# Performance work log

Measured on AMD Instinct MI355X. Metric: run time of the kernel, lower is better.

Reference implementation:

```python
import jax, jax.numpy as jnp
import numpy as np

K = 16
NS = [2048, 512, 128]

def _knn(q, r, k):
    # q: [B,M,3] query centers, r: [B,N,3] reference points -> (idx [B,M,k], sqdist [B,M,k])
    d2 = (jnp.sum(q * q, -1)[:, :, None] + jnp.sum(r * r, -1)[:, None, :]
          - 2.0 * jnp.einsum('bmd,bnd->bmn', q, r))
    neg, idx = jax.lax.top_k(-d2, k)
    return idx, jnp.maximum(-neg, 0.0)

def _gather(feat, idx):
    # feat [B,N,C], idx [B,M,k] -> [B,M,k,C]
    return jax.vmap(lambda f, i: f[i])(feat, idx)

def _down(x, pos, n, W1, b1, W2, b2):
    # PointNet++-style TransitionDown: sample n centers, kNN group, rel-pos concat, shared MLP, max-pool
    centers = pos[:, :n]
    idx, _ = _knn(centers, pos, K)
    rel = _gather(pos, idx) - centers[:, :, None, :]           # [B,n,K,3]
    feat = jnp.concatenate([rel, _gather(x, idx)], -1)          # [B,n,K,C+3]
    h = jax.nn.relu(feat @ W1 + b1) @ W2 + b2                   # last_act=False
    return jnp.max(h, axis=2), centers

def _up(xc, pc, prv_feat, prv_pos, W, b):
    # TransitionUp: 3-NN inverse-distance interpolation + skip concat + pointwise conv1d
    idx, d2 = _knn(prv_pos, pc, 3)
    w = 1.0 / (d2 + 1e-8)
    w = w / jnp.sum(w, -1, keepdims=True)
    interp = jnp.sum(_gather(xc, idx) * w[..., None], axis=2)   # [B,Nprv,Cc]
    cat = jnp.concatenate([interp, prv_feat], -1)
    return jax.nn.relu(cat @ W + b)

def setup_inputs() -> dict:
    key = jax.random.key(0)
    ks = jax.random.split(key, 16)
    p = lambda k, s: jax.random.normal(k, s, jnp.float32) * 0.02
    B, N = 4, 8192
    return {
        'x': jax.random.normal(ks[0], (B, N, 3), jnp.float32),
        'pos': jax.random.uniform(ks[1], (B, N, 3), jnp.float32),
        'd0_W1': p(ks[2], (6, 128)),   'd0_b1': jnp.zeros((128,), jnp.float32),
        'd0_W2': p(ks[3], (128, 128)), 'd0_b2': jnp.zeros((128,), jnp.float32),
        'd1_W1': p(ks[4], (131, 256)), 'd1_b1': jnp.zeros((256,), jnp.float32),
        'd1_W2': p(ks[5], (256, 256)), 'd1_b2': jnp.zeros((256,), jnp.float32),
        'd2_W1': p(ks[6], (259, 512)), 'd2_b1': jnp.zeros((512,), jnp.float32),
        'd2_W2': p(ks[7], (512, 512)), 'd2_b2': jnp.zeros((512,), jnp.float32),
        'u0_W': p(ks[8], (768, 256)),  'u0_b': jnp.zeros((256,), jnp.float32),
        'u1_W': p(ks[9], (384, 128)),  'u1_b': jnp.zeros((128,), jnp.float32),
        'u2_W': p(ks[10], (134, 128)), 'u2_b': jnp.zeros((128,), jnp.float32),
        'f_W1': p(ks[11], (128, 128)), 'f_b1': jnp.zeros((128,), jnp.float32),
        'f_W2': p(ks[12], (128, 128)), 'f_b2': jnp.zeros((128,), jnp.float32),
    }

def reference(x, pos, d0_W1, d0_b1, d0_W2, d0_b2, d1_W1, d1_b1, d1_W2, d1_b2,
              d2_W1, d2_b1, d2_W2, d2_b2, u0_W, u0_b, u1_W, u1_b, u2_W, u2_b,
              f_W1, f_b1, f_W2, f_b2):
    pos0, x0 = pos, x
    # encoder (transition-down) with cached (pos, x) per scale
    x1, pos1 = _down(x0, pos0, NS[0], d0_W1, d0_b1, d0_W2, d0_b2)
    x2, pos2 = _down(x1, pos1, NS[1], d1_W1, d1_b1, d1_W2, d1_b2)
    x3, pos3 = _down(x2, pos2, NS[2], d2_W1, d2_b1, d2_W2, d2_b2)
    # decoder (transition-up) consuming the cache in reverse; last level concats raw pos to skip feat
    up = _up(x3, pos3, x2, pos2, u0_W, u0_b)
    up = _up(up, pos2, x1, pos1, u1_W, u1_b)
    prv0 = jnp.concatenate([x0, pos0], -1)
    up = _up(up, pos1, prv0, pos0, u2_W, u2_b)
    # feat_map_layer_out: two pointwise conv1d layers, last_act=False
    out = jax.nn.relu(up @ f_W1 + f_b1) @ f_W2 + f_b2
    return (out, pos0)
```

## Files before the change

### kernel.cpp

```cpp
#include <hip/hip_runtime.h>

#define NFULL 8192
#define BATCH 4

typedef unsigned long long u64;
typedef unsigned int u32;
typedef __attribute__((ext_vector_type(8))) short bf8_t;
typedef __attribute__((ext_vector_type(4))) float f4_t;

__device__ __forceinline__ u32 fbias(float f) {
  u32 u = __float_as_uint(f);
  return (u & 0x80000000u) ? ~u : (u | 0x80000000u);
}
__device__ __forceinline__ float funbias(u32 b) {
  u32 u = (b & 0x80000000u) ? (b & 0x7fffffffu) : ~b;
  return __uint_as_float(u);
}
__device__ __forceinline__ short f2bf(float f) {
  u32 u = __float_as_uint(f);
  u32 r = u + 0x7FFFu + ((u >> 16) & 1u);
  return (short)(r >> 16);
}

__global__ __launch_bounds__(256) void build_grids_kernel(
    const float* __restrict__ pos, float4* __restrict__ sortedA,
    int* __restrict__ csA, float4* __restrict__ sortedB, int* __restrict__ csB,
    float4* __restrict__ sortedC, int* __restrict__ csC) {
  __shared__ int cnt[4096];
  __shared__ int partial[256];
  int which = blockIdx.y, b = blockIdx.x, t = threadIdx.x;
  int NREF = (which == 0) ? 8192 : (which == 1) ? 2048 : 512;
  int GR = (which == 0) ? 16 : 8;
  int NC = GR * GR * GR;
  float4* sorted = ((which == 0) ? sortedA : (which == 1) ? sortedB : sortedC)
                   + (size_t)b * NREF;
  int* cs = ((which == 0) ? csA + b * 4097 : (which == 1) ? csB + b * 513
                                           : csC + b * 513);
  const float* pb = pos + (size_t)b * NFULL * 3;
  for (int c = t; c < NC; c += 256) cnt[c] = 0;
  __syncthreads();
  for (int p = t; p < NREF; p += 256) {
    float x = pb[p * 3 + 0], y = pb[p * 3 + 1], z = pb[p * 3 + 2];
    int cx = min(max((int)(x * GR), 0), GR - 1);
    int cy = min(max((int)(y * GR), 0), GR - 1);
    int cz = min(max((int)(z * GR), 0), GR - 1);
    atomicAdd(&cnt[(cz * GR + cy) * GR + cx], 1);
  }
  __syncthreads();
  int chunk = (NC + 255) / 256;
  int s = 0;
  for (int i = 0; i < chunk; ++i) {
    int c = t * chunk + i;
    if (c < NC) s += cnt[c];
  }
  partial[t] = s;
  __syncthreads();
  if (t == 0) {
    int run = 0;
    for (int i = 0; i < 256; ++i) { int v = partial[i]; partial[i] = run; run += v; }
  }
  __syncthreads();
  int run = partial[t];
  for (int i = 0; i < chunk; ++i) {
    int c = t * chunk + i;
    if (c < NC) { int v = cnt[c]; cnt[c] = run; run += v; }
  }
  __syncthreads();
  for (int c = t; c < NC; c += 256) cs[c] = cnt[c];
  if (t == 0) cs[NC] = NREF;
  __syncthreads();
  for (int p = t; p < NREF; p += 256) {
    float x = pb[p * 3 + 0], y = pb[p * 3 + 1], z = pb[p * 3 + 2];
    int cx = min(max((int)(x * GR), 0), GR - 1);
    int cy = min(max((int)(y * GR), 0), GR - 1);
    int cz = min(max((int)(z * GR), 0), GR - 1);
    int slot = atomicAdd(&cnt[(cz * GR + cy) * GR + cx], 1);
    sorted[slot] = make_float4(x, y, z, __uint_as_float((u32)p));
  }
}

template<int SL>
__device__ __forceinline__ void group_insert(u32 m16, u64 ck, int slot,
                                             u64& val, u64& tau) {
  if (m16) {
    while (m16) {
      int src = __ffs(m16) - 1;
      m16 &= m16 - 1;
      u64 c = __shfl((unsigned long long)ck, src, 16);
      u64 prev = __shfl_up((unsigned long long)val, 1, SL);
      if (slot == 0) prev = 0ull;
      val = (val <= c) ? val : ((prev <= c) ? c : prev);
    }
    tau = __shfl((unsigned long long)val, SL - 1, SL);
  }
}

template<int SL>
__device__ __forceinline__ void first_round_sort(u64 ck, int gl,
                                                 u64& val, u64& tau) {
  u64 v = ck;
#pragma unroll
  for (int size = 2; size <= 16; size <<= 1) {
#pragma unroll
    for (int stride = size >> 1; stride > 0; stride >>= 1) {
      u64 other = __shfl_xor((unsigned long long)v, stride, 16);
      bool ddd = ((gl & size) == 0);
      bool takeMin = (((gl & stride) == 0) == ddd);
      u64 mn = (v <= other) ? v : other;
      u64 mx = (v <= other) ? other : v;
      v = takeMin ? mn : mx;
    }
  }
  if (SL < 16) v = __shfl((unsigned long long)v, gl & (SL - 1), 16);
  val = v;
  tau = __shfl((unsigned long long)v, SL - 1, SL);
}

__device__ __forceinline__ void lane_insert3(u64 ck, u64& v0, u64& v1, u64& v2) {
  u64 a = (v0 <= ck) ? v0 : ck;
  u64 bb = (v0 <= ck) ? ck : v0;
  v0 = a;
  u64 c = (v1 <= bb) ? v1 : bb;
  u64 d = (v1 <= bb) ? bb : v1;
  v1 = c;
  v2 = (v2 <= d) ? v2 : d;
}

__device__ __forceinline__ void merge3(u64 v0, u64 v1, u64 v2,
                                       u64& o0, u64& o1, u64& o2) {
  u64 h = v0;
  int hc = 0;
  u64 outs[3];
#pragma unroll
  for (int k = 0; k < 3; ++k) {
    u64 m = h;
#pragma unroll
    for (int st = 1; st < 16; st <<= 1) {
      u64 o = __shfl_xor((unsigned long long)m, st, 16);
      m = (m <= o) ? m : o;
    }
    outs[k] = m;
    if (h == m) { ++hc; h = (hc == 1) ? v1 : ((hc == 2) ? v2 : ~0ull); }
  }
  o0 = outs[0]; o1 = outs[1]; o2 = outs[2];
}

__device__ __forceinline__ void scan_range3(const float4* __restrict__ sb,
    int s, int e, float qx, float qy, float qz, float qq,
    int gl, u64& v0, u64& v1, u64& v2) {
  for (int t0 = s; t0 < e; t0 += 16) {
    int j = t0 + gl;
    if (j < e) {
      float4 P = sb[j];
      float rr = P.x * P.x + P.y * P.y + P.z * P.z;
      float d2 = qq + rr - 2.0f * (qx * P.x + qy * P.y + qz * P.z);
      u64 ck = ((u64)fbias(d2) << 32) | (u32)__float_as_uint(P.w);
      lane_insert3(ck, v0, v1, v2);
    }
  }
}

template<int SL>
__device__ __forceinline__ void scan_range(const float4* __restrict__ sb,
    int s, int e, float qx, float qy, float qz, float qq,
    int g, int gl, int slot, u64& val, u64& tau) {
  for (int t0 = s; t0 < e; t0 += 16) {
    int j = t0 + gl;
    u64 ck = ~0ull;
    if (j < e) {
      float4 P = sb[j];
      float rr = P.x * P.x + P.y * P.y + P.z * P.z;
      float d2 = qq + rr - 2.0f * (qx * P.x + qy * P.y + qz * P.z);
      ck = ((u64)fbias(d2) << 32) | (u32)__float_as_uint(P.w);
    }
    u64 full = __ballot(ck < tau);
    u32 m16 = (u32)((full >> (g * 16)) & 0xFFFFull);
    group_insert<SL>(m16, ck, slot, val, tau);
  }
}


template<int SL, int KOUT, int GR, int R, int NREF>
__device__ __forceinline__ void knn_tail(
    const float4* __restrict__ sb, const int* __restrict__ cs,
    float qx, float qy, float qz, float qq,
    int ix, int iy, int iz, int x0, int x1, int y0, int y1, int z0, int z1,
    int g, int gl, int slot, u64& val, u64& tau) {
  const float h = 1.0f / GR;
  float m = 1e30f;
  if (x0 > 0)      m = fminf(m, qx - x0 * h);
  if (x1 < GR - 1) m = fminf(m, (x1 + 1) * h - qx);
  if (y0 > 0)      m = fminf(m, qy - y0 * h);
  if (y1 < GR - 1) m = fminf(m, (y1 + 1) * h - qy);
  if (z0 > 0)      m = fminf(m, qz - z0 * h);
  if (z1 < GR - 1) m = fminf(m, (z1 + 1) * h - qz);
  float bound = m * m;
  u64 kv = __shfl((unsigned long long)val, KOUT - 1, SL);
  float kth_d2 = funbias((u32)(kv >> 32));
  if (!(kth_d2 < bound)) {
    int X0 = max(ix - (R + 1), 0), X1 = min(ix + (R + 1), GR - 1);
    int Y0 = max(iy - (R + 1), 0), Y1 = min(iy + (R + 1), GR - 1);
    int Z0 = max(iz - (R + 1), 0), Z1 = min(iz + (R + 1), GR - 1);
    int NY2 = Y1 - Y0 + 1;
    int nrow2 = (Z1 - Z0 + 1) * NY2;
    for (int rr2 = 0; rr2 < nrow2; ++rr2) {
      int zz = Z0 + rr2 / NY2, yy = Y0 + rr2 % NY2;
      int c0 = (zz * GR + yy) * GR;
      bool mid = (zz >= z0 && zz <= z1 && yy >= y0 && yy <= y1);
      int s1 = cs[c0 + X0];
      int e1 = mid ? cs[c0 + x0] : cs[c0 + X1 + 1];
      scan_range<SL>(sb, s1, e1, qx, qy, qz, qq, g, gl, slot, val, tau);
      if (mid) {
        int s2 = cs[c0 + x1 + 1];
        int e2 = cs[c0 + X1 + 1];
        scan_range<SL>(sb, s2, e2, qx, qy, qz, qq, g, gl, slot, val, tau);
      }
    }
    x0 = X0; x1 = X1; y0 = Y0; y1 = Y1; z0 = Z0; z1 = Z1;
    m = 1e30f;
    if (x0 > 0)      m = fminf(m, qx - x0 * h);
    if (x1 < GR - 1) m = fminf(m, (x1 + 1) * h - qx);
    if (y0 > 0)      m = fminf(m, qy - y0 * h);
    if (y1 < GR - 1) m = fminf(m, (y1 + 1) * h - qy);
    if (z0 > 0)      m = fminf(m, qz - z0 * h);
    if (z1 < GR - 1) m = fminf(m, (z1 + 1) * h - qz);
    bound = m * m;
    kv = __shfl((unsigned long long)val, KOUT - 1, SL);
    kth_d2 = funbias((u32)(kv >> 32));
    if (!(kth_d2 < bound)) {
      for (int t0 = 0; t0 < NREF; t0 += 16) {
        int j = t0 + gl;
        u64 ck = ~0ull;
        if (j < NREF) {
          float4 P = sb[j];
          int cx = min(max((int)(P.x * GR), 0), GR - 1);
          int cy = min(max((int)(P.y * GR), 0), GR - 1);
          int cz = min(max((int)(P.z * GR), 0), GR - 1);
          bool inbox = (cx >= x0 && cx <= x1 && cy >= y0 && cy <= y1 &&
                        cz >= z0 && cz <= z1);
          if (!inbox) {
            float rr = P.x * P.x + P.y * P.y + P.z * P.z;
            float d2 = qq + rr - 2.0f * (qx * P.x + qy * P.y + qz * P.z);
            ck = ((u64)fbias(d2) << 32) | (u32)__float_as_uint(P.w);
          }
        }
        u64 full = __ballot(ck < tau);
        u32 m16 = (u32)((full >> (g * 16)) & 0xFFFFull);
        group_insert<SL>(m16, ck, slot, val, tau);
      }
    }
  }
}

template<int GR, int R, int NREF>
__device__ __forceinline__ void knn_tail3(
    const float4* __restrict__ sb, const int* __restrict__ cs,
    float qx, float qy, float qz, float qq,
    int ix, int iy, int iz, int x0, int x1, int y0, int y1, int z0, int z1,
    int gl, u64& v0, u64& v1, u64& v2, u64& o0, u64& o1, u64& o2) {
  const float h = 1.0f / GR;
  float m = 1e30f;
  if (x0 > 0)      m = fminf(m, qx - x0 * h);
  if (x1 < GR - 1) m = fminf(m, (x1 + 1) * h - qx);
  if (y0 > 0)      m = fminf(m, qy - y0 * h);
  if (y1 < GR - 1) m = fminf(m, (y1 + 1) * h - qy);
  if (z0 > 0)      m = fminf(m, qz - z0 * h);
  if (z1 < GR - 1) m = fminf(m, (z1 + 1) * h - qz);
  float bound = m * m;
  merge3(v0, v1, v2, o0, o1, o2);
  float kth_d2 = funbias((u32)(o2 >> 32));
  if (!(kth_d2 < bound)) {
    int X0 = max(ix - (R + 1), 0), X1 = min(ix + (R + 1), GR - 1);
    int Y0 = max(iy - (R + 1), 0), Y1 = min(iy + (R + 1), GR - 1);
    int Z0 = max(iz - (R + 1), 0), Z1 = min(iz + (R + 1), GR - 1);
    int NY2 = Y1 - Y0 + 1;
    int nrow2 = (Z1 - Z0 + 1) * NY2;
    for (int rr2 = 0; rr2 < nrow2; ++rr2) {
      int zz = Z0 + rr2 / NY2, yy = Y0 + rr2 % NY2;
      int c0 = (zz * GR + yy) * GR;
      bool mid = (zz >= z0 && zz <= z1 && yy >= y0 && yy <= y1);
      int s1 = cs[c0 + X0];
      int e1 = mid ? cs[c0 + x0] : cs[c0 + X1 + 1];
// ... 203 lines not shown

__device__ void knn_brute3_dev(int vbx,
    const float* __restrict__ pos, int Nref, int Mq,
    int* __restrict__ oidx, float* __restrict__ od2) {
  int b = blockIdx.y;
  int wv = threadIdx.x >> 6, lane = threadIdx.x & 63;
  int g = lane >> 4, gl = lane & 15;
  int q = vbx * 16 + wv * 4 + g;
  const float* pb = pos + (size_t)b * NFULL * 3;
  float qx = pb[q * 3 + 0], qy = pb[q * 3 + 1], qz = pb[q * 3 + 2];
  float qq = qx * qx + qy * qy + qz * qz;

  u64 v0 = ~0ull, v1 = ~0ull, v2 = ~0ull;
  for (int j = gl; j < Nref; j += 16) {
    float rx = pb[j * 3 + 0];
    float ry = pb[j * 3 + 1];
    float rz = pb[j * 3 + 2];
    float rr = rx * rx + ry * ry + rz * rz;
    float d2 = qq + rr - 2.0f * (qx * rx + qy * ry + qz * rz);
    u64 ck = ((u64)fbias(d2) << 32) | (u32)j;
    lane_insert3(ck, v0, v1, v2);
  }
  u64 o0, o1, o2;
  merge3(v0, v1, v2, o0, o1, o2);

  if (gl < 3) {
    u64 val = (gl == 0) ? o0 : ((gl == 1) ? o1 : o2);
    size_t base = ((size_t)b * Mq + q) * 3;
    oidx[base + gl] = (int)(u32)val;
    od2[base + gl] = fmaxf(funbias((u32)(val >> 32)), 0.0f);
  }
}

template<int SL, int KOUT, int GR, int R, int NREF>
__device__ void knn_grid_flat32_dev(int vbx,
    const float* __restrict__ pos, const float4* __restrict__ sorted,
    const int* __restrict__ cellStart, int csStride, int Mq,
    int* __restrict__ oidx, float* __restrict__ od2) {
  int b = blockIdx.y;
  int wv = threadIdx.x >> 6, lane = threadIdx.x & 63;
  int g = lane >> 4, gl = lane & 15;
  int q = vbx * 16 + wv * 4 + g;
  const float* pb = pos + (size_t)b * NFULL * 3;
  const float4* sb = sorted + (size_t)b * NREF;
  const int* cs = cellStart + b * csStride;
  float qx = pb[q * 3 + 0], qy = pb[q * 3 + 1], qz = pb[q * 3 + 2];
  float qq = qx * qx + qy * qy + qz * qz;
  int ix = min(max((int)(qx * GR), 0), GR - 1);
  int iy = min(max((int)(qy * GR), 0), GR - 1);
  int iz = min(max((int)(qz * GR), 0), GR - 1);
  int x0 = max(ix - R, 0), x1 = min(ix + R, GR - 1);
  int y0 = max(iy - R, 0), y1 = min(iy + R, GR - 1);
  int z0 = max(iz - R, 0), z1 = min(iz + R, GR - 1);

  int ny = y1 - y0 + 1;
  int nrow = (z1 - z0 + 1) * ny;
  int sLo = 0, lenLo = 0, sHi = 0, lenHi = 0;
  if (gl < nrow) {
    int zz = z0 + gl / ny, yy = y0 + gl % ny;
    int c0 = (zz * GR + yy) * GR + x0;
    sLo = cs[c0]; lenLo = cs[c0 + (x1 - x0) + 1] - sLo;
  }
  {
    int i2 = gl + 16;
    if (i2 < nrow) {
      int zz = z0 + i2 / ny, yy = y0 + i2 % ny;
      int c0 = (zz * GR + yy) * GR + x0;
      sHi = cs[c0]; lenHi = cs[c0 + (x1 - x0) + 1] - sHi;
    }
  }
  int pLo = lenLo, pHi = lenHi;
#pragma unroll
  for (int st = 1; st < 16; st <<= 1) {
    int o = __shfl_up(pLo, st, 16);
    if (gl >= st) pLo += o;
    int o2 = __shfl_up(pHi, st, 16);
    if (gl >= st) pHi += o2;
  }
  int tot16 = __shfl(pLo, 15, 16);
  pHi += tot16;
  int T = __shfl(pHi, 15, 16);
  pLo -= lenLo; pHi -= lenHi;
  int dLo = sLo - pLo, dHi = sHi - pHi;
  if (gl >= nrow) pLo = 0x7fffffff;
  if (gl + 16 >= nrow) pHi = 0x7fffffff;

  int slot = gl & (SL - 1);
  u64 val, tau;

  {
    int v = gl;
    int r = 0;
#pragma unroll
    for (int st = 16; st >= 1; st >>= 1) {
      int j = r + st;
      int pcL = __shfl(pLo, j & 15, 16);
      int pcH = __shfl(pHi, j & 15, 16);
      int pc = (j < 16) ? pcL : pcH;
      if (v >= pc) r = j;
    }
    int dL = __shfl(dLo, r & 15, 16);
    int dH = __shfl(dHi, r & 15, 16);
    int addr = v + ((r < 16) ? dL : dH);
    u64 ck = ~0ull;
    if (v < T) {
      float4 P = sb[addr];
      float rr = P.x * P.x + P.y * P.y + P.z * P.z;
      float d2 = qq + rr - 2.0f * (qx * P.x + qy * P.y + qz * P.z);
      ck = ((u64)fbias(d2) << 32) | (u32)__float_as_uint(P.w);
    }
    first_round_sort<SL>(ck, gl, val, tau);
  }

  for (int v0 = 16; v0 < T; v0 += 16) {
    int v = v0 + gl;
    int r = 0;
#pragma unroll
    for (int st = 16; st >= 1; st >>= 1) {
      int j = r + st;
      int pcL = __shfl(pLo, j & 15, 16);
      int pcH = __shfl(pHi, j & 15, 16);
      int pc = (j < 16) ? pcL : pcH;
      if (v >= pc) r = j;
    }
    int dL = __shfl(dLo, r & 15, 16);
    int dH = __shfl(dHi, r & 15, 16);
    int addr = v + ((r < 16) ? dL : dH);
    u64 ck = ~0ull;
    if (v < T) {
      float4 P = sb[addr];
      float rr = P.x * P.x + P.y * P.y + P.z * P.z;
      float d2 = qq + rr - 2.0f * (qx * P.x + qy * P.y + qz * P.z);
      ck = ((u64)fbias(d2) << 32) | (u32)__float_as_uint(P.w);
    }
    u64 full = __ballot(ck < tau);
    u32 m16 = (u32)((full >> (g * 16)) & 0xFFFFull);
    group_insert<SL>(m16, ck, slot, val, tau);
  }

  knn_tail<SL, KOUT, GR, R, NREF>(sb, cs, qx, qy, qz, qq,
      ix, iy, iz, x0, x1, y0, y1, z0, z1, g, gl, slot, val, tau);

  if (gl < KOUT) {
    size_t base = ((size_t)b * Mq + q) * KOUT;
    oidx[base + gl] = (int)(u32)val;
    if (od2) od2[base + gl] = fmaxf(funbias((u32)(val >> 32)), 0.0f);
  }
}

template<int SL, int KOUT>
__device__ void knn_brute_dev(int vbx,
    const float* __restrict__ pos, int Nref, int Mq,
    int* __restrict__ oidx, float* __restrict__ od2) {
  int b = blockIdx.y;
  int wv = threadIdx.x >> 6, lane = threadIdx.x & 63;
  int g = lane >> 4, gl = lane & 15;
  int q = vbx * 16 + wv * 4 + g;
  const float* pb = pos + (size_t)b * NFULL * 3;
  float qx = pb[q * 3 + 0], qy = pb[q * 3 + 1], qz = pb[q * 3 + 2];
  float qq = qx * qx + qy * qy + qz * qz;

  int slot = gl & (SL - 1);
  u64 val, tau;

  {
    int j = gl;
    float rx = pb[j * 3 + 0];
    float ry = pb[j * 3 + 1];
    float rz = pb[j * 3 + 2];
    float rr = rx * rx + ry * ry + rz * rz;
    float d2 = qq + rr - 2.0f * (qx * rx + qy * ry + qz * rz);
    u64 ck = ((u64)fbias(d2) << 32) | (u32)j;
    first_round_sort<SL>(ck, gl, val, tau);
  }

  for (int t0 = 16; t0 < Nref; t0 += 16) {
    int j = t0 + gl;
    float rx = pb[j * 3 + 0];
    float ry = pb[j * 3 + 1];
    float rz = pb[j * 3 + 2];
    float rr = rx * rx + ry * ry + rz * rz;
    float d2 = qq + rr - 2.0f * (qx * rx + qy * ry + qz * rz);
    u64 ck = ((u64)fbias(d2) << 32) | (u32)j;
    u64 full = __ballot(ck < tau);
    u32 m16 = (u32)((full >> (g * 16)) & 0xFFFFull);
    group_insert<SL>(m16, ck, slot, val, tau);
  }

  if (gl < KOUT) {
    size_t base = ((size_t)b * Mq + q) * KOUT;
    oidx[base + gl] = (int)(u32)val;
    if (od2) od2[base + gl] = fmaxf(funbias((u32)(val >> 32)), 0.0f);
  }
}

__global__ __launch_bounds__(256) void knn_all_kernel(
    const float* __restrict__ pos,
    const float4* __restrict__ sortedA, const int* __restrict__ csA,
    const float4* __restrict__ sortedB, const int* __restrict__ csB,
    const float4* __restrict__ sortedC, const int* __restrict__ csC,
    int* __restrict__ idx0, int* __restrict__ idx1, int* __restrict__ idx2,
    int* __restrict__ idxu0, float* __restrict__ d2u0,
    int* __restrict__ idxu1, float* __restrict__ d2u1,
    int* __restrict__ idxu2, float* __restrict__ d2u2) {
  int bx = blockIdx.x;
  if (bx < 8)
    knn_brute_dev<16, 16>(bx, pos, 512, 128, idx2, nullptr);
  else if (bx < 40)
    knn_grid_flat32_dev<16, 16, 8, 2, 2048>(bx - 8, pos, sortedB, csB, 513, 512, idx1, nullptr);
  else if (bx < 168)
    knn_grid_flat32_dev<16, 16, 16, 2, 8192>(bx - 40, pos, sortedA, csA, 4097, 2048, idx0, nullptr);
  else if (bx < 296)
    knn_grid_flat32_3_dev<8, 2, 512>(bx - 168, pos, sortedC, csC, 513, 2048, idxu1, d2u1);
  else if (bx < 808)
    knn_grid_flat3_dev<8, 1, 2048>(bx - 296, pos, sortedB, csB, 513, 8192, idxu2, d2u2);
  else
    knn_brute3_dev(bx - 808, pos, 128, 512, idxu0, d2u0);
}

__device__ __forceinline__ void pack_tile_rt(const float* __restrict__ W,
                                             short* __restrict__ outp,
                                             int KDIM, int N, int tile, int lane) {
  int NT = N >> 4;
  int kt = tile / NT, nt = tile - kt * NT;
  int n = nt * 16 + (lane & 15);
  int k0 = kt * 32 + (lane >> 4) * 8;
  bf8_t v;
#pragma unroll
  for (int j = 0; j < 8; ++j) {
    int k = k0 + j;
    v[j] = (k < KDIM) ? f2bf(W[(size_t)k * N + n]) : (short)0;
  }
  *(bf8_t*)(outp + ((size_t)tile * 64 + lane) * 8) = v;
}

__global__ __launch_bounds__(64) void pack_copy_all_kernel(
    const float* d0W1, short* d0W1p, const float* d0W2, short* d0W2p,
    const float* d1W1, short* d1W1p, const float* d1W2, short* d1W2p,
    const float* d2W1, short* d2W1p, const float* d2W2, short* d2W2p,
    const float* u2W, short* u2Wp, const float* fW1, short* fW1p,
    const float* fW2, short* fW2p,
    const float* u0W, short* u0Wp, const float* u1W, short* u1Wp,
    const float* pos, float* posOut) {
  int blk = blockIdx.x, lane = threadIdx.x;
  if      (blk < 8)    pack_tile_rt(d0W1, d0W1p, 6, 128, blk, lane);
  else if (blk < 40)   pack_tile_rt(d0W2, d0W2p, 128, 128, blk - 8, lane);
  else if (blk < 120)  pack_tile_rt(d1W1, d1W1p, 131, 256, blk - 40, lane);
  else if (blk < 248)  pack_tile_rt(d1W2, d1W2p, 256, 256, blk - 120, lane);
  else if (blk < 536)  pack_tile_rt(d2W1, d2W1p, 259, 512, blk - 248, lane);
  else if (blk < 1048) pack_tile_rt(d2W2, d2W2p, 512, 512, blk - 536, lane);
  else if (blk < 1088) pack_tile_rt(u2W, u2Wp, 134, 128, blk - 1048, lane);
  else if (blk < 1120) pack_tile_rt(fW1, fW1p, 128, 128, blk - 1088, lane);
  else if (blk < 1152) pack_tile_rt(fW2, fW2p, 128, 128, blk - 1120, lane);
  else if (blk < 1536) pack_tile_rt(u0W, u0Wp, 768, 256, blk - 1152, lane);
  else if (blk < 1632) pack_tile_rt(u1W, u1Wp, 384, 128, blk - 1536, lane);
  else {
    int base = (blk - 1632) * 256;
#pragma unroll
    for (int j = 0; j < 4; ++j) {
      int i = base + lane + j * 64;
      posOut[i] = pos[i];
    }
  }
}

template<int FEAT, int CIN, int CHID, int FPAD, int QB, int WAVES>
__global__ __launch_bounds__(64 * WAVES) void down_mfma_kernel(
    const float* __restrict__ pos, const float* __restrict__ xin,
    const int* __restrict__ idx,
    const short* __restrict__ W1p, const float* __restrict__ b1,
    const short* __restrict__ W2p, const float* __restrict__ b2,
    float* __restrict__ out, int n, int nprev) {
  const int KT1 = FPAD / 32, NT1 = CHID / 16;
  const int KT2 = CHID / 32, NT2 = CHID / 16;
  __shared__ short sFeat[QB][16][FPAD + 8];
  __shared__ short sH1[QB][16][CHID + 8];
  __shared__ int sIdx[QB][16];
  __shared__ float sCtr[QB][3];
  int b = blockIdx.y, q0 = blockIdx.x * QB;
  int t = threadIdx.x;
  int lane = t & 63, wv = t >> 6;
  const float* pb = pos + (size_t)b * NFULL * 3;
  const float* xb = xin + (size_t)b * nprev * CIN;
  if (t < QB * 16)
    sIdx[t >> 4][t & 15] = idx[((size_t)b * n + q0 + (t >> 4)) * 16 + (t & 15)];
  if (t < QB * 3) sCtr[t / 3][t % 3] = pb[(q0 + t / 3) * 3 + (t % 3)];
  __syncthreads();
  for (int e = t; e < QB * 16 * FPAD; e += 64 * WAVES) {
    int k = e / FPAD, c = e - k * FPAD;
    int qq = k >> 4, kk = k & 15;
    float v = 0.f;
    if (c < 3) v = pb[sIdx[qq][kk] * 3 + c] - sCtr[qq][c];
    else if (c < FEAT) v = xb[(size_t)sIdx[qq][kk] * CIN + (c - 3)];
    sFeat[qq][kk][c] = f2bf(v);
  }
  __syncthreads();
// ... 268 lines not shown
  float* x2    = (float*)(ws + 4194304);
  float* x3    = (float*)(ws + 6291456);
  float* up0o  = (float*)(ws + 7340032);
  float* up1o  = (float*)(ws + 9437184);
  int*   idx0  = (int*)  (ws + 13631488);
  int*   idx1  = (int*)  (ws + 14155776);
  int*   idx2  = (int*)  (ws + 14286848);
  float4* sortedC = (float4*)(ws + 14319616);
  int*    csC     = (int*)   (ws + 14352384);
  int*   idxu0 = (int*)  (ws + 14843904);
  float* d2u0  = (float*)(ws + 14868480);
  int*   idxu1 = (int*)  (ws + 14893056);
  float* d2u1  = (float*)(ws + 14991360);
  int*   idxu2 = (int*)  (ws + 15089664);
  float* d2u2  = (float*)(ws + 15482880);
  short* d1W1p = (short*)(ws + 15876096);
  short* d1W2p = (short*)(ws + 15958016);
  short* d2W1p = (short*)(ws + 16089088);
  short* d2W2p = (short*)(ws + 16384000);
  short* d0W1p = (short*)(ws + 16908288);
  short* d0W2p = (short*)(ws + 16916480);
  float4* sortedA = (float4*)(ws + 16949248);
  int*    csA     = (int*)   (ws + 17473536);
  float4* sortedB = (float4*)(ws + 17539136);
  int*    csB     = (int*)   (ws + 17670208);
  short* u2Wp  = (short*)(ws + 17697920);
  short* fW1p  = (short*)(ws + 17738880);
  short* fW2p  = (short*)(ws + 17771648);

  float* out = (float*)d_out;
  short* u0Wp = (short*)out;
  short* u1Wp = (short*)(out + 98304);

  pack_copy_all_kernel<<<dim3(2016), 64, 0, stream>>>(
      d0W1, d0W1p, d0W2, d0W2p, d1W1, d1W1p, d1W2, d1W2p,
      d2W1, d2W1p, d2W2, d2W2p, u2W, u2Wp, fW1, fW1p, fW2, fW2p,
      u0W, u0Wp, u1W, u1Wp,
      pos, out + (size_t)BATCH * NFULL * 128);
  build_grids_kernel<<<dim3(BATCH, 3), 256, 0, stream>>>(
      pos, sortedA, csA, sortedB, csB, sortedC, csC);

  knn_all_kernel<<<dim3(840, BATCH), 256, 0, stream>>>(
      pos, sortedA, csA, sortedB, csB, sortedC, csC,
      idx0, idx1, idx2,
      idxu0, d2u0, idxu1, d2u1, idxu2, d2u2);

  down_mfma_kernel<6, 3, 128, 32, 4, 4><<<dim3(512, BATCH), 256, 0, stream>>>(
      pos, x, idx0, d0W1p, d0b1, d0W2p, d0b2, x1, 2048, 8192);
  down_mfma_kernel<131, 128, 256, 160, 4, 8><<<dim3(128, BATCH), 512, 0, stream>>>(
      pos, x1, idx1, d1W1p, d1b1, d1W2p, d1b2, x2, 512, 2048);
  down_mfma_kernel<259, 256, 512, 288, 2, 8><<<dim3(64, BATCH), 512, 0, stream>>>(
      pos, x2, idx2, d2W1p, d2b1, d2W2p, d2b2, x3, 128, 512);

  up_mfma_kernel<512, 256, 256, 4><<<dim3(32, BATCH), 256, 0, stream>>>(
      x3, 128, idxu0, d2u0, x2, u0Wp, u0b, up0o, 512);
  up_mfma_kernel<256, 128, 128, 2><<<dim3(128, BATCH), 128, 0, stream>>>(
      up0o, 512, idxu1, d2u1, x1, u1Wp, u1b, up1o, 2048);
  up2f_mfma_kernel<<<dim3(512, BATCH), 128, 0, stream>>>(
      up1o, idxu2, d2u2, x, pos, u2Wp, u2b, fW1p, fb1, fW2p, fb2, out);
}
```

Measured before the change: 299.9 us.

## Use 32-lane kNN groups and merge grid build with weight packing kernel

The K=16 kNN searches now give each query 32 lanes instead of 16. Each scan step therefore evaluates 32 candidates, and the per-row prefix scan spans all 32 lanes, removing the Lo/Hi split. The separate weight-pack/pos-copy kernel and grid-build kernel are fused into one pre_kernel, saving a launch. The cost is fewer queries per wave, more blocks, and potentially more serial insert iterations per ballot.

```diff
diff --git a/kernel.cpp b/kernel.cpp
--- a/kernel.cpp
+++ b/kernel.cpp
@@ -22,13 +22,74 @@
   return (short)(r >> 16);
 }
 
-__global__ __launch_bounds__(256) void build_grids_kernel(
+__device__ __forceinline__ void pack_tile_rt(const float* __restrict__ W,
+                                             short* __restrict__ outp,
+                                             int KDIM, int N, int tile, int lane) {
+  int NT = N >> 4;
+  int kt = tile / NT, nt = tile - kt * NT;
+  int n = nt * 16 + (lane & 15);
+  int k0 = kt * 32 + (lane >> 4) * 8;
+  bf8_t v;
+#pragma unroll
+  for (int j = 0; j < 8; ++j) {
+    int k = k0 + j;
+    v[j] = (k < KDIM) ? f2bf(W[(size_t)k * N + n]) : (short)0;
+  }
+  *(bf8_t*)(outp + ((size_t)tile * 64 + lane) * 8) = v;
+}
+
+__device__ void pack_dispatch(int blk, int lane,
+    const float* d0W1, short* d0W1p, const float* d0W2, short* d0W2p,
+    const float* d1W1, short* d1W1p, const float* d1W2, short* d1W2p,
+    const float* d2W1, short* d2W1p, const float* d2W2, short* d2W2p,
+    const float* u2W, short* u2Wp, const float* fW1, short* fW1p,
+    const float* fW2, short* fW2p,
+    const float* u0W, short* u0Wp, const float* u1W, short* u1Wp,
+    const float* pos, float* posOut) {
+  if      (blk < 8)    pack_tile_rt(d0W1, d0W1p, 6, 128, blk, lane);
+  else if (blk < 40)   pack_tile_rt(d0W2, d0W2p, 128, 128, blk - 8, lane);
+  else if (blk < 120)  pack_tile_rt(d1W1, d1W1p, 131, 256, blk - 40, lane);
+  else if (blk < 248)  pack_tile_rt(d1W2, d1W2p, 256, 256, blk - 120, lane);
+  else if (blk < 536)  pack_tile_rt(d2W1, d2W1p, 259, 512, blk - 248, lane);
+  else if (blk < 1048) pack_tile_rt(d2W2, d2W2p, 512, 512, blk - 536, lane);
+  else if (blk < 1088) pack_tile_rt(u2W, u2Wp, 134, 128, blk - 1048, lane);
+  else if (blk < 1120) pack_tile_rt(fW1, fW1p, 128, 128, blk - 1088, lane);
+  else if (blk < 1152) pack_tile_rt(fW2, fW2p, 128, 128, blk - 1120, lane);
+  else if (blk < 1536) pack_tile_rt(u0W, u0Wp, 768, 256, blk - 1152, lane);
+  else if (blk < 1632) pack_tile_rt(u1W, u1Wp, 384, 128, blk - 1536, lane);
+  else {
+    int base = (blk - 1632) * 256;
+#pragma unroll
+    for (int j = 0; j < 4; ++j) {
+      int i = base + lane + j * 64;
+      posOut[i] = pos[i];
+    }
+  }
+}
+
+__global__ __launch_bounds__(256) void pre_kernel(
     const float* __restrict__ pos, float4* __restrict__ sortedA,
     int* __restrict__ csA, float4* __restrict__ sortedB, int* __restrict__ csB,
-    float4* __restrict__ sortedC, int* __restrict__ csC) {
+    float4* __restrict__ sortedC, int* __restrict__ csC,
+    const float* d0W1, short* d0W1p, const float* d0W2, short* d0W2p,
+    const float* d1W1, short* d1W1p, const float* d1W2, short* d1W2p,
+    const float* d2W1, short* d2W1p, const float* d2W2, short* d2W2p,
+    const float* u2W, short* u2Wp, const float* fW1, short* fW1p,
+    const float* fW2, short* fW2p,
+    const float* u0W, short* u0Wp, const float* u1W, short* u1Wp,
+    float* posOut) {
   __shared__ int cnt[4096];
   __shared__ int partial[256];
-  int which = blockIdx.y, b = blockIdx.x, t = threadIdx.x;
+  int bx = blockIdx.x, t = threadIdx.x;
+  if (bx >= 12) {
+    int tt = (bx - 12) * 4 + (t >> 6);
+    pack_dispatch(tt, t & 63,
+        d0W1, d0W1p, d0W2, d0W2p, d1W1, d1W1p, d1W2, d1W2p,
+        d2W1, d2W1p, d2W2, d2W2p, u2W, u2Wp, fW1, fW1p, fW2, fW2p,
+        u0W, u0Wp, u1W, u1Wp, pos, posOut);
+    return;
+  }
+  int which = bx >> 2, b = bx & 3;
   int NREF = (which == 0) ? 8192 : (which == 1) ? 2048 : 512;
   int GR = (which == 0) ? 16 : 8;
   int NC = GR * GR * GR;
@@ -79,31 +140,29 @@
   }
 }
 
-template<int SL>
-__device__ __forceinline__ void group_insert(u32 m16, u64 ck, int slot,
-                                             u64& val, u64& tau) {
-  if (m16) {
-    while (m16) {
-      int src = __ffs(m16) - 1;
-      m16 &= m16 - 1;
-      u64 c = __shfl((unsigned long long)ck, src, 16);
-      u64 prev = __shfl_up((unsigned long long)val, 1, SL);
-      if (slot == 0) prev = 0ull;
+__device__ __forceinline__ void group_insert_g32(u32 m32, u64 ck, int slot16,
+                                                 u64& val, u64& tau) {
+  if (m32) {
+    while (m32) {
+      int src = __ffs(m32) - 1;
+      m32 &= m32 - 1;
+      u64 c = __shfl((unsigned long long)ck, src, 32);
+      u64 prev = __shfl_up((unsigned long long)val, 1, 16);
+      if (slot16 == 0) prev = 0ull;
       val = (val <= c) ? val : ((prev <= c) ? c : prev);
     }
-    tau = __shfl((unsigned long long)val, SL - 1, SL);
-  }
-}
-
-template<int SL>
-__device__ __forceinline__ void first_round_sort(u64 ck, int gl,
-                                                 u64& val, u64& tau) {
+    tau = __shfl((unsigned long long)val, 15, 16);
+  }
+}
+
+__device__ __forceinline__ void first_round_sort32(u64 ck, int gl,
+                                                   u64& val, u64& tau) {
   u64 v = ck;
 #pragma unroll
-  for (int size = 2; size <= 16; size <<= 1) {
+  for (int size = 2; size <= 32; size <<= 1) {
 #pragma unroll
     for (int stride = size >> 1; stride > 0; stride >>= 1) {
-      u64 other = __shfl_xor((unsigned long long)v, stride, 16);
+      u64 other = __shfl_xor((unsigned long long)v, stride, 32);
       bool ddd = ((gl & size) == 0);
       bool takeMin = (((gl & stride) == 0) == ddd);
       u64 mn = (v <= other) ? v : other;
@@ -111,60 +170,14 @@
       v = takeMin ? mn : mx;
     }
   }
-  if (SL < 16) v = __shfl((unsigned long long)v, gl & (SL - 1), 16);
-  val = v;
-  tau = __shfl((unsigned long long)v, SL - 1, SL);
-}
-
-__device__ __forceinline__ void lane_insert3(u64 ck, u64& v0, u64& v1, u64& v2) {
-  u64 a = (v0 <= ck) ? v0 : ck;
-  u64 bb = (v0 <= ck) ? ck : v0;
-  v0 = a;
-  u64 c = (v1 <= bb) ? v1 : bb;
-  u64 d = (v1 <= bb) ? bb : v1;
-  v1 = c;
-  v2 = (v2 <= d) ? v2 : d;
-}
-
-__device__ __forceinline__ void merge3(u64 v0, u64 v1, u64 v2,
-                                       u64& o0, u64& o1, u64& o2) {
-  u64 h = v0;
-  int hc = 0;
-  u64 outs[3];
-#pragma unroll
-  for (int k = 0; k < 3; ++k) {
-    u64 m = h;
-#pragma unroll
-    for (int st = 1; st < 16; st <<= 1) {
-      u64 o = __shfl_xor((unsigned long long)m, st, 16);
-      m = (m <= o) ? m : o;
-    }
-    outs[k] = m;
-    if (h == m) { ++hc; h = (hc == 1) ? v1 : ((hc == 2) ? v2 : ~0ull); }
-  }
-  o0 = outs[0]; o1 = outs[1]; o2 = outs[2];
-}
-
-__device__ __forceinline__ void scan_range3(const float4* __restrict__ sb,
+  val = __shfl((unsigned long long)v, gl & 15, 32);
+  tau = __shfl((unsigned long long)val, 15, 16);
+}
+
+__device__ __forceinline__ void scan_range_g32(const float4* __restrict__ sb,
     int s, int e, float qx, float qy, float qz, float qq,
-    int gl, u64& v0, u64& v1, u64& v2) {
-  for (int t0 = s; t0 < e; t0 += 16) {
-    int j = t0 + gl;
-    if (j < e) {
-      float4 P = sb[j];
-      float rr = P.x * P.x + P.y * P.y + P.z * P.z;
-      float d2 = qq + rr - 2.0f * (qx * P.x + qy * P.y + qz * P.z);
-      u64 ck = ((u64)fbias(d2) << 32) | (u32)__float_as_uint(P.w);
-      lane_insert3(ck, v0, v1, v2);
-    }
-  }
-}
-
-template<int SL>
-__device__ __forceinline__ void scan_range(const float4* __restrict__ sb,
-    int s, int e, float qx, float qy, float qz, float qq,
-    int g, int gl, int slot, u64& val, u64& tau) {
-  for (int t0 = s; t0 < e; t0 += 16) {
+    int g32, int gl, int slot16, u64& val, u64& tau) {
+  for (int t0 = s; t0 < e; t0 += 32) {
     int j = t0 + gl;
     u64 ck = ~0ull;
     if (j < e) {
@@ -174,18 +187,17 @@
       ck = ((u64)fbias(d2) << 32) | (u32)__float_as_uint(P.w);
     }
     u64 full = __ballot(ck < tau);
-    u32 m16 = (u32)((full >> (g * 16)) & 0xFFFFull);
-    group_insert<SL>(m16, ck, slot, val, tau);
-  }
-}
-
-
-template<int SL, int KOUT, int GR, int R, int NREF>
-__device__ __forceinline__ void knn_tail(
+    u32 m32 = (u32)(full >> (g32 * 32));
+    group_insert_g32(m32, ck, slot16, val, tau);
+  }
+}
+
+template<int GR, int R, int NREF>
+__device__ __forceinline__ void knn_tail16_g32(
     const float4* __restrict__ sb, const int* __restrict__ cs,
     float qx, float qy, float qz, float qq,
     int ix, int iy, int iz, int x0, int x1, int y0, int y1, int z0, int z1,
-    int g, int gl, int slot, u64& val, u64& tau) {
+    int g32, int gl, int slot16, u64& val, u64& tau) {
   const float h = 1.0f / GR;
   float m = 1e30f;
   if (x0 > 0)      m = fminf(m, qx - x0 * h);
@@ -195,8 +207,7 @@
   if (z0 > 0)      m = fminf(m, qz - z0 * h);
   if (z1 < GR - 1) m = fminf(m, (z1 + 1) * h - qz);
   float bound = m * m;
-  u64 kv = __shfl((unsigned long long)val, KOUT - 1, SL);
-  float kth_d2 = funbias((u32)(kv >> 32));
+  float kth_d2 = funbias((u32)(tau >> 32));
   if (!(kth_d2 < bound)) {
     int X0 = max(ix - (R + 1), 0), X1 = min(ix + (R + 1), GR - 1);
     int Y0 = max(iy - (R + 1), 0), Y1 = min(iy + (R + 1), GR - 1);
@@ -209,11 +220,11 @@
       bool mid = (zz >= z0 && zz <= z1 && yy >= y0 && yy <= y1);
       int s1 = cs[c0 + X0];
       int e1 = mid ? cs[c0 + x0] : cs[c0 + X1 + 1];
-      scan_range<SL>(sb, s1, e1, qx, qy, qz, qq, g, gl, slot, val, tau);
+      scan_range_g32(sb, s1, e1, qx, qy, qz, qq, g32, gl, slot16, val, tau);
       if (mid) {
         int s2 = cs[c0 + x1 + 1];
         int e2 = cs[c0 + X1 + 1];
-        scan_range<SL>(sb, s2, e2, qx, qy, qz, qq, g, gl, slot, val, tau);
+        scan_range_g32(sb, s2, e2, qx, qy, qz, qq, g32, gl, slot16, val, tau);
       }
     }
     x0 = X0; x1 = X1; y0 = Y0; y1 = Y1; z0 = Z0; z1 = Z1;
@@ -225,10 +236,9 @@
     if (z0 > 0)      m = fminf(m, qz - z0 * h);
     if (z1 < GR - 1) m = fminf(m, (z1 + 1) * h - qz);
     bound = m * m;
-    kv = __shfl((unsigned long long)val, KOUT - 1, SL);
-    kth_d2 = funbias((u32)(kv >> 32));
+    kth_d2 = funbias((u32)(tau >> 32));
     if (!(kth_d2 < bound)) {
-      for (int t0 = 0; t0 < NREF; t0 += 16) {
+      for (int t0 = 0; t0 < NREF; t0 += 32) {
         int j = t0 + gl;
         u64 ck = ~0ull;
         if (j < NREF) {
@@ -245,9 +255,189 @@
           }
         }
         u64 full = __ballot(ck < tau);
-        u32 m16 = (u32)((full >> (g * 16)) & 0xFFFFull);
-        group_insert<SL>(m16, ck, slot, val, tau);
+        u32 m32 = (u32)(full >> (g32 * 32));
+        group_insert_g32(m32, ck, slot16, val, tau);
       }
+    }
+  }
+}
+
+template<int GR, int R, int NREF>
+__device__ void knn_grid16_g32_dev(int vbx,
+    const float* __restrict__ pos, const float4* __restrict__ sorted,
+    const int* __restrict__ cellStart, int csStride, int Mq,
+    int* __restrict__ oidx) {
+  int b = blockIdx.y;
+  int wv = threadIdx.x >> 6, lane = threadIdx.x & 63;
+  int g32 = lane >> 5, gl = lane & 31;
+  int q = vbx * 8 + wv * 2 + g32;
+  const float* pb = pos + (size_t)b * NFULL * 3;
+  const float4* sb = sorted + (size_t)b * NREF;
+  const int* cs = cellStart + b * csStride;
+  float qx = pb[q * 3 + 0], qy = pb[q * 3 + 1], qz = pb[q * 3 + 2];
+  float qq = qx * qx + qy * qy + qz * qz;
+  int ix = min(max((int)(qx * GR), 0), GR - 1);
+  int iy = min(max((int)(qy * GR), 0), GR - 1);
+  int iz = min(max((int)(qz * GR), 0), GR - 1);
+  int x0 = max(ix - R, 0), x1 = min(ix + R, GR - 1);
+  int y0 = max(iy - R, 0), y1 = min(iy + R, GR - 1);
+  int z0 = max(iz - R, 0), z1 = min(iz + R, GR - 1);
+
+  int ny = y1 - y0 + 1;
+  int nrow = (z1 - z0 + 1) * ny;
+  int s_i = 0, len_i = 0;
+  if (gl < nrow) {
+    int zz = z0 + gl / ny, yy = y0 + gl % ny;
+    int c0 = (zz * GR + yy) * GR + x0;
+    s_i = cs[c0];
+    len_i = cs[c0 + (x1 - x0) + 1] - s_i;
+  }
+  int p_i = len_i;
+#pragma unroll
+  for (int st = 1; st < 32; st <<= 1) {
+    int o = __shfl_up(p_i, st, 32);
+    if (gl >= st) p_i += o;
+  }
+  int T = __shfl(p_i, 31, 32);
+  p_i -= len_i;
+  int d_i = s_i - p_i;
+  if (gl >= nrow) p_i = 0x7fffffff;
+
+  int slot16 = lane & 15;
+  u64 val, tau;
+
+  {
+    int v = gl;
+    int r = 0;
+#pragma unroll
+    for (int st = 16; st >= 1; st >>= 1) {
+      int pc = __shfl(p_i, r + st, 32);
+      if (v >= pc) r += st;
+    }
+    int addr = v + __shfl(d_i, r, 32);
+    u64 ck = ~0ull;
+    if (v < T) {
+      float4 P = sb[addr];
+      float rr = P.x * P.x + P.y * P.y + P.z * P.z;
+      float d2 = qq + rr - 2.0f * (qx * P.x + qy * P.y + qz * P.z);
+      ck = ((u64)fbias(d2) << 32) | (u32)__float_as_uint(P.w);
+    }
+    first_round_sort32(ck, gl, val, tau);
+  }
+
+  for (int v0 = 32; v0 < T; v0 += 32) {
+    int v = v0 + gl;
+    int r = 0;
+#pragma unroll
+    for (int st = 16; st >= 1; st >>= 1) {
+      int pc = __shfl(p_i, r + st, 32);
+      if (v >= pc) r += st;
+    }
+    int addr = v + __shfl(d_i, r, 32);
+    u64 ck = ~0ull;
+    if (v < T) {
+      float4 P = sb[addr];
+      float rr = P.x * P.x + P.y * P.y + P.z * P.z;
+      float d2 = qq + rr - 2.0f * (qx * P.x + qy * P.y + qz * P.z);
+      ck = ((u64)fbias(d2) << 32) | (u32)__float_as_uint(P.w);
+    }
+    u64 full = __ballot(ck < tau);
+    u32 m32 = (u32)(full >> (g32 * 32));
+    group_insert_g32(m32, ck, slot16, val, tau);
+  }
+
+  knn_tail16_g32<GR, R, NREF>(sb, cs, qx, qy, qz, qq,
+      ix, iy, iz, x0, x1, y0, y1, z0, z1, g32, gl, slot16, val, tau);
+
+  if (gl < 16) {
+    size_t base = ((size_t)b * Mq + q) * 16;
+    oidx[base + gl] = (int)(u32)val;
+  }
+}
+
+__device__ void knn_brute16_g32_dev(int vbx,
+    const float* __restrict__ pos, int Nref, int Mq, int* __restrict__ oidx) {
+  int b = blockIdx.y;
+  int wv = threadIdx.x >> 6, lane = threadIdx.x & 63;
+  int g32 = lane >> 5, gl = lane & 31;
+  int q = vbx * 8 + wv * 2 + g32;
+  const float* pb = pos + (size_t)b * NFULL * 3;
+  float qx = pb[q * 3 + 0], qy = pb[q * 3 + 1], qz = pb[q * 3 + 2];
+  float qq = qx * qx + qy * qy + qz * qz;
+
+  int slot16 = lane & 15;
+  u64 val, tau;
+
+  {
+    int j = gl;
+    float rx = pb[j * 3 + 0];
+    float ry = pb[j * 3 + 1];
+    float rz = pb[j * 3 + 2];
+    float rr = rx * rx + ry * ry + rz * rz;
+    float d2 = qq + rr - 2.0f * (qx * rx + qy * ry + qz * rz);
+    u64 ck = ((u64)fbias(d2) << 32) | (u32)j;
+    first_round_sort32(ck, gl, val, tau);
+  }
+
+  for (int t0 = 32; t0 < Nref; t0 += 32) {
+    int j = t0 + gl;
+    float rx = pb[j * 3 + 0];
+    float ry = pb[j * 3 + 1];
+    float rz = pb[j * 3 + 2];
+    float rr = rx * rx + ry * ry + rz * rz;
+    float d2 = qq + rr - 2.0f * (qx * rx + qy * ry + qz * rz);
+    u64 ck = ((u64)fbias(d2) << 32) | (u32)j;
+    u64 full = __ballot(ck < tau);
+    u32 m32 = (u32)(full >> (g32 * 32));
+    group_insert_g32(m32, ck, slot16, val, tau);
+  }
+
+  if (gl < 16) {
+    size_t base = ((size_t)b * Mq + q) * 16;
+    oidx[base + gl] = (int)(u32)val;
+  }
+}
+
+__device__ __forceinline__ void lane_insert3(u64 ck, u64& v0, u64& v1, u64& v2) {
+  u64 a = (v0 <= ck) ? v0 : ck;
+  u64 bb = (v0 <= ck) ? ck : v0;
+  v0 = a;
+  u64 c = (v1 <= bb) ? v1 : bb;
+  u64 d = (v1 <= bb) ? bb : v1;
+  v1 = c;
+  v2 = (v2 <= d) ? v2 : d;
+}
+
+__device__ __forceinline__ void merge3(u64 v0, u64 v1, u64 v2,
+                                       u64& o0, u64& o1, u64& o2) {
+  u64 h = v0;
+  int hc = 0;
+  u64 outs[3];
+#pragma unroll
+  for (int k = 0; k < 3; ++k) {
+    u64 m = h;
+#pragma unroll
+    for (int st = 1; st < 16; st <<= 1) {
+      u64 o = __shfl_xor((unsigned long long)m, st, 16);
+      m = (m <= o) ? m : o;
+    }
+    outs[k] = m;
+    if (h == m) { ++hc; h = (hc == 1) ? v1 : ((hc == 2) ? v2 : ~0ull); }
+  }
+  o0 = outs[0]; o1 = outs[1]; o2 = outs[2];
+}
+
+__device__ __forceinline__ void scan_range3(const float4* __restrict__ sb,
+    int s, int e, float qx, float qy, float qz, float qq,
+    int gl, u64& v0, u64& v1, u64& v2) {
+  for (int t0 = s; t0 < e; t0 += 16) {
+    int j = t0 + gl;
+    if (j < e) {
+      float4 P = sb[j];
+      float rr = P.x * P.x + P.y * P.y + P.z * P.z;
+      float d2 = qq + rr - 2.0f * (qx * P.x + qy * P.y + qz * P.z);
+      u64 ck = ((u64)fbias(d2) << 32) | (u32)__float_as_uint(P.w);
+      lane_insert3(ck, v0, v1, v2);
     }
   }
 }
@@ -517,168 +707,6 @@
   }
 }
 
-template<int SL, int KOUT, int GR, int R, int NREF>
-__device__ void knn_grid_flat32_dev(int vbx,
-    const float* __restrict__ pos, const float4* __restrict__ sorted,
-    const int* __restrict__ cellStart, int csStride, int Mq,
-    int* __restrict__ oidx, float* __restrict__ od2) {
-  int b = blockIdx.y;
-  int wv = threadIdx.x >> 6, lane = threadIdx.x & 63;
-  int g = lane >> 4, gl = lane & 15;
-  int q = vbx * 16 + wv * 4 + g;
-  const float* pb = pos + (size_t)b * NFULL * 3;
-  const float4* sb = sorted + (size_t)b * NREF;
-  const int* cs = cellStart + b * csStride;
-  float qx = pb[q * 3 + 0], qy = pb[q * 3 + 1], qz = pb[q * 3 + 2];
-  float qq = qx * qx + qy * qy + qz * qz;
-  int ix = min(max((int)(qx * GR), 0), GR - 1);
-  int iy = min(max((int)(qy * GR), 0), GR - 1);
-  int iz = min(max((int)(qz * GR), 0), GR - 1);
-  int x0 = max(ix - R, 0), x1 = min(ix + R, GR - 1);
-  int y0 = max(iy - R, 0), y1 = min(iy + R, GR - 1);
-  int z0 = max(iz - R, 0), z1 = min(iz + R, GR - 1);
-
-  int ny = y1 - y0 + 1;
-  int nrow = (z1 - z0 + 1) * ny;
-  int sLo = 0, lenLo = 0, sHi = 0, lenHi = 0;
-  if (gl < nrow) {
-    int zz = z0 + gl / ny, yy = y0 + gl % ny;
-    int c0 = (zz * GR + yy) * GR + x0;
-    sLo = cs[c0]; lenLo = cs[c0 + (x1 - x0) + 1] - sLo;
-  }
-  {
-    int i2 = gl + 16;
-    if (i2 < nrow) {
-      int zz = z0 + i2 / ny, yy = y0 + i2 % ny;
-      int c0 = (zz * GR + yy) * GR + x0;
-      sHi = cs[c0]; lenHi = cs[c0 + (x1 - x0) + 1] - sHi;
-    }
-  }
-  int pLo = lenLo, pHi = lenHi;
-#pragma unroll
-  for (int st = 1; st < 16; st <<= 1) {
-    int o = __shfl_up(pLo, st, 16);
-    if (gl >= st) pLo += o;
-    int o2 = __shfl_up(pHi, st, 16);
-    if (gl >= st) pHi += o2;
-  }
-  int tot16 = __shfl(pLo, 15, 16);
-  pHi += tot16;
-  int T = __shfl(pHi, 15, 16);
-  pLo -= lenLo; pHi -= lenHi;
-  int dLo = sLo - pLo, dHi = sHi - pHi;
-  if (gl >= nrow) pLo = 0x7fffffff;
-  if (gl + 16 >= nrow) pHi = 0x7fffffff;
-
-  int slot = gl & (SL - 1);
-  u64 val, tau;
-
-  {
-    int v = gl;
-    int r = 0;
-#pragma unroll
-    for (int st = 16; st >= 1; st >>= 1) {
-      int j = r + st;
-      int pcL = __shfl(pLo, j & 15, 16);
-      int pcH = __shfl(pHi, j & 15, 16);
-      int pc = (j < 16) ? pcL : pcH;
-      if (v >= pc) r = j;
-    }
-    int dL = __shfl(dLo, r & 15, 16);
-    int dH = __shfl(dHi, r & 15, 16);
-    int addr = v + ((r < 16) ? dL : dH);
-    u64 ck = ~0ull;
-    if (v < T) {
-      float4 P = sb[addr];
-      float rr = P.x * P.x + P.y * P.y + P.z * P.z;
-      float d2 = qq + rr - 2.0f * (qx * P.x + qy * P.y + qz * P.z);
-      ck = ((u64)fbias(d2) << 32) | (u32)__float_as_uint(P.w);
-    }
-    first_round_sort<SL>(ck, gl, val, tau);
-  }
-
-  for (int v0 = 16; v0 < T; v0 += 16) {
-    int v = v0 + gl;
-    int r = 0;
-#pragma unroll
-    for (int st = 16; st >= 1; st >>= 1) {
-      int j = r + st;
-      int pcL = __shfl(pLo, j & 15, 16);
-      int pcH = __shfl(pHi, j & 15, 16);
-      int pc = (j < 16) ? pcL : pcH;
-      if (v >= pc) r = j;
-    }
-    int dL = __shfl(dLo, r & 15, 16);
-    int dH = __shfl(dHi, r & 15, 16);
-    int addr = v + ((r < 16) ? dL : dH);
-    u64 ck = ~0ull;
-    if (v < T) {
-      float4 P = sb[addr];
-      float rr = P.x * P.x + P.y * P.y + P.z * P.z;
-      float d2 = qq + rr - 2.0f * (qx * P.x + qy * P.y + qz * P.z);
-      ck = ((u64)fbias(d2) << 32) | (u32)__float_as_uint(P.w);
-    }
-    u64 full = __ballot(ck < tau);
-    u32 m16 = (u32)((full >> (g * 16)) & 0xFFFFull);
-    group_insert<SL>(m16, ck, slot, val, tau);
-  }
-
-  knn_tail<SL, KOUT, GR, R, NREF>(sb, cs, qx, qy, qz, qq,
-      ix, iy, iz, x0, x1, y0, y1, z0, z1, g, gl, slot, val, tau);
-
-  if (gl < KOUT) {
-    size_t base = ((size_t)b * Mq + q) * KOUT;
-    oidx[base + gl] = (int)(u32)val;
-    if (od2) od2[base + gl] = fmaxf(funbias((u32)(val >> 32)), 0.0f);
-  }
-}
-
-template<int SL, int KOUT>
-__device__ void knn_brute_dev(int vbx,
-    const float* __restrict__ pos, int Nref, int Mq,
-    int* __restrict__ oidx, float* __restrict__ od2) {
-  int b = blockIdx.y;
-  int wv = threadIdx.x >> 6, lane = threadIdx.x & 63;
-  int g = lane >> 4, gl = lane & 15;
-  int q = vbx * 16 + wv * 4 + g;
-  const float* pb = pos + (size_t)b * NFULL * 3;
-  float qx = pb[q * 3 + 0], qy = pb[q * 3 + 1], qz = pb[q * 3 + 2];
-  float qq = qx * qx + qy * qy + qz * qz;
-
-  int slot = gl & (SL - 1);
-  u64 val, tau;
-
-  {
-    int j = gl;
-    float rx = pb[j * 3 + 0];
-    float ry = pb[j * 3 + 1];
-    float rz = pb[j * 3 + 2];
-    float rr = rx * rx + ry * ry + rz * rz;
-    float d2 = qq + rr - 2.0f * (qx * rx + qy * ry + qz * rz);
-    u64 ck = ((u64)fbias(d2) << 32) | (u32)j;
-    first_round_sort<SL>(ck, gl, val, tau);
-  }
-
-  for (int t0 = 16; t0 < Nref; t0 += 16) {
-    int j = t0 + gl;
-    float rx = pb[j * 3 + 0];
-    float ry = pb[j * 3 + 1];
-    float rz = pb[j * 3 + 2];
-    float rr = rx * rx + ry * ry + rz * rz;
-    float d2 = qq + rr - 2.0f * (qx * rx + qy * ry + qz * rz);
-    u64 ck = ((u64)fbias(d2) << 32) | (u32)j;
-    u64 full = __ballot(ck < tau);
-    u32 m16 = (u32)((full >> (g * 16)) & 0xFFFFull);
-    group_insert<SL>(m16, ck, slot, val, tau);
-  }
-
-  if (gl < KOUT) {
-    size_t base = ((size_t)b * Mq + q) * KOUT;
-    oidx[base + gl] = (int)(u32)val;
-    if (od2) od2[base + gl] = fmaxf(funbias((u32)(val >> 32)), 0.0f);
-  }
-}
-
 __global__ __launch_bounds__(256) void knn_all_kernel(
     const float* __restrict__ pos,
     const float4* __restrict__ sortedA, const int* __restrict__ csA,
@@ -689,64 +717,18 @@
     int* __restrict__ idxu1, float* __restrict__ d2u1,
     int* __restrict__ idxu2, float* __restrict__ d2u2) {
   int bx = blockIdx.x;
-  if (bx < 8)
-    knn_brute_dev<16, 16>(bx, pos, 512, 128, idx2, nullptr);
-  else if (bx < 40)
-    knn_grid_flat32_dev<16, 16, 8, 2, 2048>(bx - 8, pos, sortedB, csB, 513, 512, idx1, nullptr);
-  else if (bx < 168)
-    knn_grid_flat32_dev<16, 16, 16, 2, 8192>(bx - 40, pos, sortedA, csA, 4097, 2048, idx0, nullptr);
-  else if (bx < 296)
-    knn_grid_flat32_3_dev<8, 2, 512>(bx - 168, pos, sortedC, csC, 513, 2048, idxu1, d2u1);
-  else if (bx < 808)
-    knn_grid_flat3_dev<8, 1, 2048>(bx - 296, pos, sortedB, csB, 513, 8192, idxu2, d2u2);
+  if (bx < 16)
+    knn_brute16_g32_dev(bx, pos, 512, 128, idx2);
+  else if (bx < 80)
+    knn_grid16_g32_dev<8, 2, 2048>(bx - 16, pos, sortedB, csB, 513, 512, idx1);
+  else if (bx < 336)
+    knn_grid16_g32_dev<16, 2, 8192>(bx - 80, pos, sortedA, csA, 4097, 2048, idx0);
+  else if (bx < 464)
+    knn_grid_flat32_3_dev<8, 2, 512>(bx - 336, pos, sortedC, csC, 513, 2048, idxu1, d2u1);
+  else if (bx < 976)
+    knn_grid_flat3_dev<8, 1, 2048>(bx - 464, pos, sortedB, csB, 513, 8192, idxu2, d2u2);
   else
-    knn_brute3_dev(bx - 808, pos, 128, 512, idxu0, d2u0);
-}
-
-__device__ __forceinline__ void pack_tile_rt(const float* __restrict__ W,
-                                             short* __restrict__ outp,
-                                             int KDIM, int N, int tile, int lane) {
-  int NT = N >> 4;
-  int kt = tile / NT, nt = tile - kt * NT;
-  int n = nt * 16 + (lane & 15);
-  int k0 = kt * 32 + (lane >> 4) * 8;
-  bf8_t v;
-#pragma unroll
-  for (int j = 0; j < 8; ++j) {
-    int k = k0 + j;
-    v[j] = (k < KDIM) ? f2bf(W[(size_t)k * N + n]) : (short)0;
-  }
-  *(bf8_t*)(outp + ((size_t)tile * 64 + lane) * 8) = v;
-}
-
-__global__ __launch_bounds__(64) void pack_copy_all_kernel(
-    const float* d0W1, short* d0W1p, const float* d0W2, short* d0W2p,
-    const float* d1W1, short* d1W1p, const float* d1W2, short* d1W2p,
-    const float* d2W1, short* d2W1p, const float* d2W2, short* d2W2p,
-    const float* u2W, short* u2Wp, const float* fW1, short* fW1p,
-    const float* fW2, short* fW2p,
-    const float* u0W, short* u0Wp, const float* u1W, short* u1Wp,
-    const float* pos, float* posOut) {
-  int blk = blockIdx.x, lane = threadIdx.x;
-  if      (blk < 8)    pack_tile_rt(d0W1, d0W1p, 6, 128, blk, lane);
-  else if (blk < 40)   pack_tile_rt(d0W2, d0W2p, 128, 128, blk - 8, lane);
-  else if (blk < 120)  pack_tile_rt(d1W1, d1W1p, 131, 256, blk - 40, lane);
-  else if (blk < 248)  pack_tile_rt(d1W2, d1W2p, 256, 256, blk - 120, lane);
-  else if (blk < 536)  pack_tile_rt(d2W1, d2W1p, 259, 512, blk - 248, lane);
-  else if (blk < 1048) pack_tile_rt(d2W2, d2W2p, 512, 512, blk - 536, lane);
-  else if (blk < 1088) pack_tile_rt(u2W, u2Wp, 134, 128, blk - 1048, lane);
-  else if (blk < 1120) pack_tile_rt(fW1, fW1p, 128, 128, blk - 1088, lane);
-  else if (blk < 1152) pack_tile_rt(fW2, fW2p, 128, 128, blk - 1120, lane);
-  else if (blk < 1536) pack_tile_rt(u0W, u0Wp, 768, 256, blk - 1152, lane);
-  else if (blk < 1632) pack_tile_rt(u1W, u1Wp, 384, 128, blk - 1536, lane);
-  else {
-    int base = (blk - 1632) * 256;
-#pragma unroll
-    for (int j = 0; j < 4; ++j) {
-      int i = base + lane + j * 64;
-      posOut[i] = pos[i];
-    }
-  }
+    knn_brute3_dev(bx - 976, pos, 128, 512, idxu0, d2u0);
 }
 
 template<int FEAT, int CIN, int CHID, int FPAD, int QB, int WAVES>
@@ -1081,15 +1063,14 @@
   short* u0Wp = (short*)out;
   short* u1Wp = (short*)(out + 98304);
 
-  pack_copy_all_kernel<<<dim3(2016), 64, 0, stream>>>(
+  pre_kernel<<<dim3(516), 256, 0, stream>>>(
+      pos, sortedA, csA, sortedB, csB, sortedC, csC,
       d0W1, d0W1p, d0W2, d0W2p, d1W1, d1W1p, d1W2, d1W2p,
       d2W1, d2W1p, d2W2, d2W2p, u2W, u2Wp, fW1, fW1p, fW2, fW2p,
       u0W, u0Wp, u1W, u1Wp,
-      pos, out + (size_t)BATCH * NFULL * 128);
-  build_grids_kernel<<<dim3(BATCH, 3), 256, 0, stream>>>(
-      pos, sortedA, csA, sortedB, csB, sortedC, csC);
-
-  knn_all_kernel<<<dim3(840, BATCH), 256, 0, stream>>>(
+      out + (size_t)BATCH * NFULL * 128);
+
+  knn_all_kernel<<<dim3(1008, BATCH), 256, 0, stream>>>(
       pos, sortedA, csA, sortedB, csB, sortedC, csC,
       idx0, idx1, idx2,
       idxu0, d2u0, idxu1, d2u1, idxu2, d2u2);
```

New measurement: 290.1 us. 3.2% less time.
